# Performance work log

Measured on AMD Instinct MI355X. Metric: run time of the kernel, lower is better.

The kernel has to match this reference:

```python
import jax, jax.numpy as jnp
import numpy as np

B, H, HKV, D, DV, S, M, BN = 16, 32, 8, 128, 128, 8192, 64, 64


def setup_inputs() -> dict:
    key = jax.random.key(0)
    k1, k2, k3, k4 = jax.random.split(key, 4)
    query = jax.random.normal(k1, (B, H, D), dtype=jnp.float32)
    K = jax.random.normal(k2, (B, S, HKV, D), dtype=jnp.float32)
    V = jax.random.normal(k3, (B, S, HKV, DV), dtype=jnp.float32)
    # selected KV block ids per (batch, kv_head); -1 would mean 'skip block'
    block_indices = jax.random.randint(k4, (B, HKV, M), 0, S // BN).astype(jnp.int32)
    cache_seqlens = jnp.full((B,), S, dtype=jnp.int32)
    return {"query": query, "key": K, "value": V,
            "block_indices": block_indices, "cache_seqlens": cache_seqlens,
            "block_size": BN}


def reference(query, key, value, block_indices, cache_seqlens, block_size):
    # query: [B,H,D]  key: [B,S,HKV,D]  value: [B,S,HKV,DV]
    # block_indices: [B,HKV,M] int32 (-1 = invalid)  cache_seqlens: [B] int32
    Bb, Hh, Dd = query.shape
    _, Ss, Hkv, Dv = value.shape
    G = Hh // Hkv  # GQA group size
    scale = 1.0 / np.sqrt(Dd).astype(np.float32)

    valid_blk = block_indices >= 0                              # [B,HKV,M]
    idx = jnp.where(valid_blk, block_indices, 0)
    pos4 = idx[..., None] * block_size + jnp.arange(block_size)  # [B,HKV,M,bn]
    mask4 = valid_blk[..., None] & (pos4 < cache_seqlens[:, None, None, None])
    pos = pos4.reshape(Bb, Hkv, -1)                              # [B,HKV,N] N=M*bn
    mask = mask4.reshape(Bb, Hkv, -1)

    # gather selected KV blocks per (batch, kv_head)
    Kt = key.transpose(0, 2, 1, 3)    # [B,HKV,S,D]
    Vt = value.transpose(0, 2, 1, 3)  # [B,HKV,S,DV]
    Kg = jnp.take_along_axis(Kt, pos[..., None], axis=2)  # [B,HKV,N,D]
    Vg = jnp.take_along_axis(Vt, pos[..., None], axis=2)  # [B,HKV,N,DV]

    q = query.reshape(Bb, Hkv, G, Dd)                      # [B,HKV,G,D]
    s = jnp.einsum('bhgd,bhnd->bhgn', q, Kg) * scale       # [B,HKV,G,N]
    s = jnp.where(mask[:, :, None, :], s, -jnp.inf)
    p = jax.nn.softmax(s, axis=-1)                         # online-softmax equiv.
    o = jnp.einsum('bhgn,bhnd->bhgd', p, Vg)               # [B,HKV,G,DV]
    return o.reshape(Bb, Hh, Dv)
```

## Files before the change

kernel.cpp:

```cpp
#include <hip/hip_runtime.h>
#include <math.h>

#define B_    16
#define H_    32
#define HKV_  8
#define G_    4
#define D_    128
#define DV_   128
#define S_    8192
#define M_    64
#define BN_   64
#define KVSTRIDE (HKV_ * D_)

#define CHUNK_ 32
#define NBLK_  4
#define SPLIT_ (M_ / NBLK_)
#define ITEMS_ 4
#define NCTOT_ (ITEMS_ * NBLK_ * 2)

__device__ __forceinline__ void gload_lds16(const float* gsrc, float* lds_dst) {
    __builtin_amdgcn_global_load_lds(
        (const __attribute__((address_space(1))) void*)gsrc,
        (__attribute__((address_space(3))) void*)lds_dst,
        16, 0, 0);
}

__device__ __forceinline__ float bcast_lane(float v, int srclane) {
    return __uint_as_float(__builtin_amdgcn_readlane(__float_as_uint(v), srclane));
}

__global__ __launch_bounds__(256)
void sfa_partial(const float* __restrict__ q,
                 const float* __restrict__ K,
                 const float* __restrict__ V,
                 const int*   __restrict__ blk_idx,
                 const int*   __restrict__ seqlens,
                 float* __restrict__ o_ws,
                 float* __restrict__ ml_ws)
{
    __shared__ float Klds[2][CHUNK_ * D_];
    __shared__ float Vlds[2][CHUNK_ * DV_];

    const int w    = blockIdx.x;
    const int t    = w >> 3;
    const int bh   = (w & 7) + 8 * (t & 15);
    const int quad = t >> 4;
    const int hkv  = bh & 7;
    const int b    = bh >> 3;

    const int tid  = threadIdx.x;
    const int wave = tid >> 6;
    const int lane = tid & 63;
    const int c    = lane & 3;
    const int jr   = lane >> 2;

    const int h = hkv * G_ + wave;
    const float kscale = 0.08838834764831845f * 1.4426950408889634f;

    float4 q4[8];
    {
        const float* qp = q + (size_t)(b * H_ + h) * D_ + c * 4;
        #pragma unroll
        for (int f = 0; f < 8; ++f) {
            float4 tq = *(const float4*)(qp + f * 16);
            q4[f] = make_float4(tq.x * kscale, tq.y * kscale,
                                tq.z * kscale, tq.w * kscale);
        }
    }

    int vblk = 0;
    if (lane < 16) vblk = blk_idx[bh * M_ + quad * 16 + lane];

    const int seqlen = seqlens[b];
    const float* Kb = K + (size_t)b * S_ * KVSTRIDE + hkv * D_;
    const float* Vb = V + (size_t)b * S_ * KVSTRIDE + hkv * D_;

    asm volatile("s_waitcnt vmcnt(0)" ::: "memory");

    auto stageK = [&](int cc, int blk) {
        const int blkc = (blk < 0) ? 0 : blk;
        const size_t rowbase = (size_t)blkc * BN_ + (cc & 1) * CHUNK_;
        float* dst = &Klds[cc & 1][0];
        #pragma unroll
        for (int i = 0; i < 4; ++i) {
            const int p   = wave * 4 + i;
            const int row = 2 * p + (lane >> 5);
            const int g16 = lane & 31;
            const float* src = Kb + (rowbase + row) * KVSTRIDE
                                  + ((g16 ^ (row & 7)) << 2);
            gload_lds16(src, dst + p * 256);
        }
    };
    auto stageV = [&](int cc, int blk) {
        const int blkc = (blk < 0) ? 0 : blk;
        const size_t rowbase = (size_t)blkc * BN_ + (cc & 1) * CHUNK_;
        float* dst = &Vlds[cc & 1][0];
        #pragma unroll
        for (int i = 0; i < 4; ++i) {
            const int p   = wave * 4 + i;
            const int row = 2 * p + (lane >> 5);
            const int g16 = lane & 31;
            const float* src = Vb + (rowbase + row) * KVSTRIDE + (g16 << 2);
            gload_lds16(src, dst + p * 256);
        }
    };
    auto blkOf = [&](int cc) -> int {
        return __builtin_amdgcn_readlane(vblk, cc >> 1);
    };

    float m  = -INFINITY;
    float l  = 0.f;
    float o0 = 0.f, o1 = 0.f;

    stageK(0, blkOf(0));
    stageV(0, blkOf(0));
    stageK(1, blkOf(1));

    #pragma unroll 1
    for (int item = 0; item < ITEMS_; ++item) {
        #pragma unroll
        for (int ci = 0; ci < 8; ++ci) {
            const int  cc   = item * 8 + ci;
            const int  blk  = blkOf(cc);
            const bool bval = (blk >= 0);
            const int  pos0 = ((blk < 0) ? 0 : blk) * BN_ + (cc & 1) * CHUNK_;
            const bool last = (cc == NCTOT_ - 1);

            if (last) asm volatile("s_waitcnt vmcnt(4)" ::: "memory");
            else      asm volatile("s_waitcnt vmcnt(8)" ::: "memory");
            __builtin_amdgcn_s_barrier();
            __builtin_amdgcn_sched_barrier(0);

            float s[2];
            #pragma unroll
            for (int bt = 0; bt < 2; ++bt) {
                const int r = bt * 16 + jr;
                const float* kr = &Klds[cc & 1][r * D_];
                float acc = 0.f;
                #pragma unroll
                for (int f = 0; f < 8; ++f) {
                    const int gg = (((f * 4 + c) ^ (r & 7)) << 2);
                    float4 k4 = *(const float4*)(kr + gg);
                    acc += q4[f].x * k4.x;
                    acc += q4[f].y * k4.y;
                    acc += q4[f].z * k4.z;
                    acc += q4[f].w * k4.w;
                }
                acc += __shfl_xor(acc, 1);
                acc += __shfl_xor(acc, 2);
                s[bt] = (bval && (pos0 + r) < seqlen) ? acc : -INFINITY;
            }

            if (cc + 1 < NCTOT_) stageV(cc + 1, blkOf(cc + 1));

            if (last) asm volatile("s_waitcnt vmcnt(0)" ::: "memory");
            else      asm volatile("s_waitcnt vmcnt(8)" ::: "memory");
            __builtin_amdgcn_s_barrier();
            __builtin_amdgcn_sched_barrier(0);

            if (cc + 2 < NCTOT_) stageK(cc + 2, blkOf(cc + 2));

            float bmax = fmaxf(s[0], s[1]);
            #pragma unroll
            for (int off = 4; off < 64; off <<= 1)
                bmax = fmaxf(bmax, __shfl_xor(bmax, off));

            const float newm = fmaxf(m, bmax);
            if (newm != -INFINITY) {
                const float rr = __builtin_amdgcn_exp2f(m - newm);
                const float p0 = __builtin_amdgcn_exp2f(s[0] - newm);
                const float p1 = __builtin_amdgcn_exp2f(s[1] - newm);
                float ps = p0 + p1;
                #pragma unroll
                for (int off = 4; off < 64; off <<= 1)
                    ps += __shfl_xor(ps, off);

                l  = l * rr + ps;
                o0 *= rr;
                o1 *= rr;
                m  = newm;

                const float* vp0 = &Vlds[cc & 1][lane * 2];
                #pragma unroll
                for (int jj = 0; jj < 16; ++jj) {
                    const float pj = bcast_lane(p0, jj * 4);
                    const float2 v2 = *(const float2*)(vp0 + jj * DV_);
                    o0 += pj * v2.x;
                    o1 += pj * v2.y;
                }
                #pragma unroll
                for (int jj = 0; jj < 16; ++jj) {
                    const float pj = bcast_lane(p1, jj * 4);
                    const float2 v2 = *(const float2*)(vp0 + (16 + jj) * DV_);
                    o0 += pj * v2.x;
                    o1 += pj * v2.y;
                }
            }

            if (ci == 7) {
                const int sp   = quad * ITEMS_ + item;
                const int pidx = (bh * G_ + wave) * SPLIT_ + sp;
                *(float2*)(o_ws + (size_t)pidx * DV_ + lane * 2) =
                    make_float2(o0, o1);
                if (lane == 0)
                    *(float2*)(ml_ws + pidx * 2) = make_float2(m, l);
                m = -INFINITY; l = 0.f; o0 = 0.f; o1 = 0.f;
            }
        }
    }
}

template<int SPLIT>
__global__ __launch_bounds__(64)
void sfa_reduce(const float* __restrict__ o_ws,
                const float* __restrict__ ml_ws,
                float* __restrict__ out)
{
    const int bhg  = blockIdx.x;
    const int lane = threadIdx.x;

    float mi = -INFINITY, li = 0.f;
    if (lane < SPLIT) {
        const float2 t = ((const float2*)ml_ws)[bhg * SPLIT + lane];
        mi = t.x; li = t.y;
    }
    float mfull = mi;
    #pragma unroll
    for (int off = 1; off < 64; off <<= 1)
        mfull = fmaxf(mfull, __shfl_xor(mfull, off));

    const float f = (mi == -INFINITY) ? 0.f
                  : __builtin_amdgcn_exp2f(mi - mfull);
    float L = li * f;
    #pragma unroll
    for (int off = 1; off < 64; off <<= 1)
        L += __shfl_xor(L, off);

    float o0 = 0.f, o1 = 0.f;
    #pragma unroll
    for (int i = 0; i < SPLIT; ++i) {
        const float fi = bcast_lane(f, i);
        if (fi != 0.f) {
            const float* op = o_ws + (size_t)(bhg * SPLIT + i) * DV_ + lane * 2;
            o0 += fi * op[0];
            o1 += fi * op[1];
        }
    }
    const float inv = (L > 0.f) ? (1.f / L) : 0.f;
    out[(size_t)bhg * DV_ + lane * 2]     = o0 * inv;
    out[(size_t)bhg * DV_ + lane * 2 + 1] = o1 * inv;
}

extern "C" void kernel_launch(void* const* d_in, const int* in_sizes, int n_in,
                              void* d_out, int out_size, void* d_ws, size_t ws_size,
                              hipStream_t stream) {
    const float* q    = (const float*)d_in[0];
    const float* K    = (const float*)d_in[1];
    const float* V    = (const float*)d_in[2];
    const int*   bidx = (const int*)d_in[3];
    const int*   slen = (const int*)d_in[4];

    float* o_ws  = (float*)d_ws;
    float* ml_ws = o_ws + (size_t)B_ * HKV_ * G_ * SPLIT_ * DV_;

    sfa_partial<<<B_ * HKV_ * SPLIT_ / ITEMS_, 256, 0, stream>>>(
        q, K, V, bidx, slen, o_ws, ml_ws);

    sfa_reduce<SPLIT_><<<B_ * H_, 64, 0, stream>>>(o_ws, ml_ws, (float*)d_out);
}
```

Measured before the change: 93.64 us.

## Shrink KV chunk to 16 rows and give each workgroup one 8-block split

Reworks the split-KV partition. Each workgroup now processes one split of 8 KV blocks in 16-row chunks with a single flat pipelined loop, instead of four 4-block items in 32-row chunks. The grid grows from 512 to 1024 workgroups, the reduce kernel merges 8 partials instead of 16, and LDS per workgroup is halved, aiming for more occupancy and less partial-result traffic. In exchange each workgroup carries more synchronisation per row of KV and does less work per barrier.

```diff
diff --git a/kernel.cpp b/kernel.cpp
--- a/kernel.cpp
+++ b/kernel.cpp
@@ -12,11 +12,10 @@
 #define BN_   64
 #define KVSTRIDE (HKV_ * D_)
 
-#define CHUNK_ 32
-#define NBLK_  4
-#define SPLIT_ (M_ / NBLK_)
-#define ITEMS_ 4
-#define NCTOT_ (ITEMS_ * NBLK_ * 2)
+#define CHUNK_ 16
+#define NBPW_  8
+#define SPLIT_ (M_ / NBPW_)
+#define NCTOT_ (NBPW_ * BN_ / CHUNK_)
 
 __device__ __forceinline__ void gload_lds16(const float* gsrc, float* lds_dst) {
     __builtin_amdgcn_global_load_lds(
@@ -42,11 +41,11 @@
     __shared__ float Vlds[2][CHUNK_ * DV_];
 
     const int w    = blockIdx.x;
+    const int hkv  = w & 7;
     const int t    = w >> 3;
-    const int bh   = (w & 7) + 8 * (t & 15);
-    const int quad = t >> 4;
-    const int hkv  = bh & 7;
-    const int b    = bh >> 3;
+    const int b    = t & 15;
+    const int oct  = t >> 4;
+    const int bh   = b * HKV_ + hkv;
 
     const int tid  = threadIdx.x;
     const int wave = tid >> 6;
@@ -69,7 +68,7 @@
     }
 
     int vblk = 0;
-    if (lane < 16) vblk = blk_idx[bh * M_ + quad * 16 + lane];
+    if (lane < NBPW_) vblk = blk_idx[bh * M_ + oct * NBPW_ + lane];
 
     const int seqlen = seqlens[b];
     const float* Kb = K + (size_t)b * S_ * KVSTRIDE + hkv * D_;
@@ -79,11 +78,11 @@
 
     auto stageK = [&](int cc, int blk) {
         const int blkc = (blk < 0) ? 0 : blk;
-        const size_t rowbase = (size_t)blkc * BN_ + (cc & 1) * CHUNK_;
+        const size_t rowbase = (size_t)blkc * BN_ + (cc & 3) * CHUNK_;
         float* dst = &Klds[cc & 1][0];
         #pragma unroll
-        for (int i = 0; i < 4; ++i) {
-            const int p   = wave * 4 + i;
+        for (int i = 0; i < 2; ++i) {
+            const int p   = wave * 2 + i;
             const int row = 2 * p + (lane >> 5);
             const int g16 = lane & 31;
             const float* src = Kb + (rowbase + row) * KVSTRIDE
@@ -93,11 +92,11 @@
     };
     auto stageV = [&](int cc, int blk) {
         const int blkc = (blk < 0) ? 0 : blk;
-        const size_t rowbase = (size_t)blkc * BN_ + (cc & 1) * CHUNK_;
+        const size_t rowbase = (size_t)blkc * BN_ + (cc & 3) * CHUNK_;
         float* dst = &Vlds[cc & 1][0];
         #pragma unroll
-        for (int i = 0; i < 4; ++i) {
-            const int p   = wave * 4 + i;
+        for (int i = 0; i < 2; ++i) {
+            const int p   = wave * 2 + i;
             const int row = 2 * p + (lane >> 5);
             const int g16 = lane & 31;
             const float* src = Vb + (rowbase + row) * KVSTRIDE + (g16 << 2);
@@ -105,7 +104,7 @@
         }
     };
     auto blkOf = [&](int cc) -> int {
-        return __builtin_amdgcn_readlane(vblk, cc >> 1);
+        return __builtin_amdgcn_readlane(vblk, cc >> 2);
     };
 
     float m  = -INFINITY;
@@ -116,98 +115,79 @@
     stageV(0, blkOf(0));
     stageK(1, blkOf(1));
 
-    #pragma unroll 1
-    for (int item = 0; item < ITEMS_; ++item) {
-        #pragma unroll
-        for (int ci = 0; ci < 8; ++ci) {
-            const int  cc   = item * 8 + ci;
-            const int  blk  = blkOf(cc);
-            const bool bval = (blk >= 0);
-            const int  pos0 = ((blk < 0) ? 0 : blk) * BN_ + (cc & 1) * CHUNK_;
-            const bool last = (cc == NCTOT_ - 1);
-
-            if (last) asm volatile("s_waitcnt vmcnt(4)" ::: "memory");
-            else      asm volatile("s_waitcnt vmcnt(8)" ::: "memory");
-            __builtin_amdgcn_s_barrier();
-            __builtin_amdgcn_sched_barrier(0);
-
-            float s[2];
+    #pragma unroll 2
+    for (int cc = 0; cc < NCTOT_; ++cc) {
+        const int  blk  = blkOf(cc);
+        const bool bval = (blk >= 0);
+        const int  pos0 = ((blk < 0) ? 0 : blk) * BN_ + (cc & 3) * CHUNK_;
+        const bool last = (cc == NCTOT_ - 1);
+
+        if (last) asm volatile("s_waitcnt vmcnt(2)" ::: "memory");
+        else      asm volatile("s_waitcnt vmcnt(4)" ::: "memory");
+        __builtin_amdgcn_s_barrier();
+        __builtin_amdgcn_sched_barrier(0);
+
+        float s0;
+        {
+            const float* kr = &Klds[cc & 1][jr * D_];
+            float acc = 0.f;
             #pragma unroll
-            for (int bt = 0; bt < 2; ++bt) {
-                const int r = bt * 16 + jr;
-                const float* kr = &Klds[cc & 1][r * D_];
-                float acc = 0.f;
-                #pragma unroll
-                for (int f = 0; f < 8; ++f) {
-                    const int gg = (((f * 4 + c) ^ (r & 7)) << 2);
-                    float4 k4 = *(const float4*)(kr + gg);
-                    acc += q4[f].x * k4.x;
-                    acc += q4[f].y * k4.y;
-                    acc += q4[f].z * k4.z;
-                    acc += q4[f].w * k4.w;
-                }
-                acc += __shfl_xor(acc, 1);
-                acc += __shfl_xor(acc, 2);
-                s[bt] = (bval && (pos0 + r) < seqlen) ? acc : -INFINITY;
+            for (int f = 0; f < 8; ++f) {
+                const int gg = (((f * 4 + c) ^ (jr & 7)) << 2);
+                float4 k4 = *(const float4*)(kr + gg);
+                acc += q4[f].x * k4.x;
+                acc += q4[f].y * k4.y;
+                acc += q4[f].z * k4.z;
+                acc += q4[f].w * k4.w;
             }
-
-            if (cc + 1 < NCTOT_) stageV(cc + 1, blkOf(cc + 1));
-
-            if (last) asm volatile("s_waitcnt vmcnt(0)" ::: "memory");
-            else      asm volatile("s_waitcnt vmcnt(8)" ::: "memory");
-            __builtin_amdgcn_s_barrier();
-            __builtin_amdgcn_sched_barrier(0);
-
-            if (cc + 2 < NCTOT_) stageK(cc + 2, blkOf(cc + 2));
-
-            float bmax = fmaxf(s[0], s[1]);
+            acc += __shfl_xor(acc, 1);
+            acc += __shfl_xor(acc, 2);
+            s0 = (bval && (pos0 + jr) < seqlen) ? acc : -INFINITY;
+        }
+
+        if (cc + 1 < NCTOT_) stageV(cc + 1, blkOf(cc + 1));
+
+        if (last) asm volatile("s_waitcnt vmcnt(0)" ::: "memory");
+        else      asm volatile("s_waitcnt vmcnt(4)" ::: "memory");
+        __builtin_amdgcn_s_barrier();
+        __builtin_amdgcn_sched_barrier(0);
+
+        if (cc + 2 < NCTOT_) stageK(cc + 2, blkOf(cc + 2));
+
+        float bmax = s0;
+        #pragma unroll
+        for (int off = 4; off < 64; off <<= 1)
+            bmax = fmaxf(bmax, __shfl_xor(bmax, off));
+
+        const float newm = fmaxf(m, bmax);
+        if (newm != -INFINITY) {
+            const float rr = __builtin_amdgcn_exp2f(m - newm);
+            const float p0 = __builtin_amdgcn_exp2f(s0 - newm);
+            float ps = p0;
             #pragma unroll
             for (int off = 4; off < 64; off <<= 1)
-                bmax = fmaxf(bmax, __shfl_xor(bmax, off));
-
-            const float newm = fmaxf(m, bmax);
-            if (newm != -INFINITY) {
-                const float rr = __builtin_amdgcn_exp2f(m - newm);
-                const float p0 = __builtin_amdgcn_exp2f(s[0] - newm);
-                const float p1 = __builtin_amdgcn_exp2f(s[1] - newm);
-                float ps = p0 + p1;
-                #pragma unroll
-                for (int off = 4; off < 64; off <<= 1)
-                    ps += __shfl_xor(ps, off);
-
-                l  = l * rr + ps;
-                o0 *= rr;
-                o1 *= rr;
-                m  = newm;
-
-                const float* vp0 = &Vlds[cc & 1][lane * 2];
-                #pragma unroll
-                for (int jj = 0; jj < 16; ++jj) {
-                    const float pj = bcast_lane(p0, jj * 4);
-                    const float2 v2 = *(const float2*)(vp0 + jj * DV_);
-                    o0 += pj * v2.x;
-                    o1 += pj * v2.y;
-                }
-                #pragma unroll
-                for (int jj = 0; jj < 16; ++jj) {
-                    const float pj = bcast_lane(p1, jj * 4);
-                    const float2 v2 = *(const float2*)(vp0 + (16 + jj) * DV_);
-                    o0 += pj * v2.x;
-                    o1 += pj * v2.y;
-                }
+                ps += __shfl_xor(ps, off);
+
+            l  = l * rr + ps;
+            o0 *= rr;
+            o1 *= rr;
+            m  = newm;
+
+            const float* vp0 = &Vlds[cc & 1][lane * 2];
+            #pragma unroll
+            for (int jj = 0; jj < 16; ++jj) {
+                const float pj = bcast_lane(p0, jj * 4);
+                const float2 v2 = *(const float2*)(vp0 + jj * DV_);
+                o0 += pj * v2.x;
+                o1 += pj * v2.y;
             }
-
-            if (ci == 7) {
-                const int sp   = quad * ITEMS_ + item;
-                const int pidx = (bh * G_ + wave) * SPLIT_ + sp;
-                *(float2*)(o_ws + (size_t)pidx * DV_ + lane * 2) =
-                    make_float2(o0, o1);
-                if (lane == 0)
-                    *(float2*)(ml_ws + pidx * 2) = make_float2(m, l);
-                m = -INFINITY; l = 0.f; o0 = 0.f; o1 = 0.f;
-            }
-        }
-    }
+        }
+    }
+
+    const int pidx = (bh * G_ + wave) * SPLIT_ + oct;
+    *(float2*)(o_ws + (size_t)pidx * DV_ + lane * 2) = make_float2(o0, o1);
+    if (lane == 0)
+        *(float2*)(ml_ws + pidx * 2) = make_float2(m, l);
 }
 
 template<int SPLIT>
@@ -263,7 +243,7 @@
     float* o_ws  = (float*)d_ws;
     float* ml_ws = o_ws + (size_t)B_ * HKV_ * G_ * SPLIT_ * DV_;
 
-    sfa_partial<<<B_ * HKV_ * SPLIT_ / ITEMS_, 256, 0, stream>>>(
+    sfa_partial<<<B_ * HKV_ * SPLIT_, 256, 0, stream>>>(
         q, K, V, bidx, slen, o_ws, ml_ws);
 
     sfa_reduce<SPLIT_><<<B_ * H_, 64, 0, stream>>>(o_ws, ml_ws, (float*)d_out);
```

Result: faster. 88.74 us (median of 2 runs) (-5.2%).
